# Optimization experiments

Hardware: AMD Instinct MI355X
Metric: run time of the kernel (lower is better)

Reference implementation:

```python
import jax, jax.numpy as jnp
import numpy as np

RES = 16          # grid resolution per axis -> num_models = 4096
L_XYZ = 10        # xyz positional-encoding frequencies -> input_ch = 63
L_DIR = 4         # dir positional-encoding frequencies -> input_ch_views = 27
W = 32
N_RAYS, N_SAMPLES = 1024, 128
NM = RES * RES * RES


def _embed(x, L):
    # NeRF frequency encoding: [x, sin(2^k x), cos(2^k x)] for k in 0..L-1
    freqs = 2.0 ** jnp.arange(L, dtype=x.dtype)          # (L,)
    xf = x[..., None, :] * freqs[:, None]                # (N, L, 3)
    enc = jnp.concatenate([jnp.sin(xf), jnp.cos(xf)], axis=-1)
    return jnp.concatenate([x, enc.reshape(x.shape[0], -1)], axis=-1)


def setup_inputs() -> dict:
    key = jax.random.key(0)
    ks = jax.random.split(key, 16)
    s = 0.05
    pts = jax.random.uniform(ks[0], (N_RAYS, N_SAMPLES, 3), dtype=jnp.float32)
    vd = jax.random.normal(ks[1], (N_RAYS, 3), dtype=jnp.float32)
    vd = vd / jnp.linalg.norm(vd, axis=-1, keepdims=True)
    return {
        "pts": pts,
        "viewdirs": vd,
        "pts_w0": s * jax.random.normal(ks[2], (NM, W, 63), dtype=jnp.float32),
        "pts_b0": s * jax.random.normal(ks[3], (NM, W), dtype=jnp.float32),
        "pts_w1": s * jax.random.normal(ks[4], (NM, W, W), dtype=jnp.float32),
        "pts_b1": s * jax.random.normal(ks[5], (NM, W), dtype=jnp.float32),
        "feat_w": s * jax.random.normal(ks[6], (NM, W, W), dtype=jnp.float32),
        "feat_b": s * jax.random.normal(ks[7], (NM, W), dtype=jnp.float32),
        "sigma_w": s * jax.random.normal(ks[8], (NM, 1, W), dtype=jnp.float32),
        "sigma_b": s * jax.random.normal(ks[9], (NM, 1), dtype=jnp.float32),
        "view_w": s * jax.random.normal(ks[10], (NM, W, W + 27), dtype=jnp.float32),
        "view_b": s * jax.random.normal(ks[11], (NM, W), dtype=jnp.float32),
        "rgb_w": s * jax.random.normal(ks[12], (NM, 3, W), dtype=jnp.float32),
        "rgb_b": s * jax.random.normal(ks[13], (NM, 3), dtype=jnp.float32),
    }


def reference(pts, viewdirs, pts_w0, pts_b0, pts_w1, pts_b1, feat_w, feat_b,
              sigma_w, sigma_b, view_w, view_b, rgb_w, rgb_b):
    n_rays, n_samples, _ = pts.shape
    p = pts.reshape(-1, 3)                                        # (N, 3)
    v = jnp.broadcast_to(viewdirs[:, None, :],
                         (n_rays, n_samples, 3)).reshape(-1, 3)   # (N, 3)

    # voxel index (aabb = [0,1]^3)
    scaled = jnp.clip(p * RES, 0.0, RES - 1.0)
    i3 = scaled.astype(jnp.int32)
    idx = i3[:, 0] * (RES * RES) + i3[:, 1] * RES + i3[:, 2]      # (N,)

    ep = _embed(p, L_XYZ)                                         # (N, 63)
    ev = _embed(v, L_DIR)                                         # (N, 27)

    # per-point tiny MLP with gathered weights: h @ w^T + b
    h = jax.nn.relu(jnp.einsum('nd,nod->no', ep, pts_w0[idx]) + pts_b0[idx])
    h = jax.nn.relu(jnp.einsum('nd,nod->no', h, pts_w1[idx]) + pts_b1[idx])

    sigma = jnp.einsum('nd,nod->no', h, sigma_w[idx]) + sigma_b[idx]   # (N, 1)
    feat = jnp.einsum('nd,nod->no', h, feat_w[idx]) + feat_b[idx]      # (N, W)

    h2 = jnp.concatenate([feat, ev], axis=-1)                          # (N, W+27)
    h2 = jax.nn.relu(jnp.einsum('nd,nod->no', h2, view_w[idx]) + view_b[idx])
    rgb = jnp.einsum('nd,nod->no', h2, rgb_w[idx]) + rgb_b[idx]        # (N, 3)

    out = jnp.concatenate([rgb, sigma], axis=-1).reshape(n_rays, n_samples, 4)
    return out[..., :3], out[..., 3:4]
```

## Files before the change

kernel.cpp:

```cpp
#include <hip/hip_runtime.h>

#define NM    4096
#define NPTS  131072
#define CAP   128

typedef _Float16 h8 __attribute__((ext_vector_type(8)));
typedef _Float16 h2 __attribute__((ext_vector_type(2)));
typedef float    f4 __attribute__((ext_vector_type(4)));
typedef int      i4 __attribute__((ext_vector_type(4)));

#define MF(a, b, c) __builtin_amdgcn_mfma_f32_16x16x32_f16((a), (b), (c), 0, 0, 0)

#if __has_builtin(__builtin_amdgcn_global_load_lds)
#define USE_DMA 1
#else
#define USE_DMA 0
#endif

static __device__ inline h2 pk(float a, float b) {
    return __builtin_bit_cast(h2, __builtin_amdgcn_cvt_pkrtz(a, b));
}

static __device__ inline h8 pack8(float u0, float u1, float u2, float u3,
                                  float u4, float u5, float u6, float u7) {
    i4 t;
    t[0] = __builtin_bit_cast(int, pk(u0, u1));
    t[1] = __builtin_bit_cast(int, pk(u2, u3));
    t[2] = __builtin_bit_cast(int, pk(u4, u5));
    t[3] = __builtin_bit_cast(int, pk(u6, u7));
    return __builtin_bit_cast(h8, t);
}

static __device__ inline h8 lds_row8(const float* __restrict__ X, int base,
                                     int d0, int lim) {
    float u[8];
    #pragma unroll
    for (int jj = 0; jj < 8; jj++) {
        int d = d0 + jj;
        float raw = X[base + d];
        u[jj] = (d < lim) ? raw : 0.f;
    }
    return pack8(u[0], u[1], u[2], u[3], u[4], u[5], u[6], u[7]);
}

static __device__ inline h8 lds_row8a(const float* __restrict__ X, int off) {
    f4 v0 = *(const f4*)(X + off);
    f4 v1 = *(const f4*)(X + off + 4);
    return pack8(v0[0], v0[1], v0[2], v0[3], v1[0], v1[1], v1[2], v1[3]);
}

static __device__ inline h8 load_row8(const float* __restrict__ rb, int d0, int lim) {
    float u[8];
    #pragma unroll
    for (int jj = 0; jj < 8; jj++) {
        int d = d0 + jj;
        u[jj] = (d < lim) ? rb[d] : 0.f;
    }
    return pack8(u[0], u[1], u[2], u[3], u[4], u[5], u[6], u[7]);
}

static __device__ inline float encdim(int d, int lim, float x, float y, float z) {
    int tt = d - 3;
    int k  = tt / 6;
    int r  = tt - 6 * k;
    float p = x;
    p = (r == 1 || r == 4) ? y : p;
    p = (r == 2 || r == 5) ? z : p;
    float f   = __int_as_float((k + 127) << 23);
    float arg = p * f + ((r >= 3) ? 1.57079632679f : 0.f);
    float sv  = __sinf(arg);
    float raw = (d == 0) ? x : ((d == 1) ? y : z);
    float val = (d < 3) ? raw : sv;
    return (d < lim) ? val : 0.f;
}

static __device__ inline h8 makeB(f4 d0, f4 d1, int quad, int col) {
    int laneA = ((quad & 1) * 2) * 16 + col;
    int laneB = laneA + 16;
    float a0 = __shfl(d0[0], laneA), b0 = __shfl(d1[0], laneA);
    float a1 = __shfl(d0[1], laneA), b1 = __shfl(d1[1], laneA);
    float a2 = __shfl(d0[2], laneA), b2 = __shfl(d1[2], laneA);
    float a3 = __shfl(d0[3], laneA), b3 = __shfl(d1[3], laneA);
    float a4 = __shfl(d0[0], laneB), b4 = __shfl(d1[0], laneB);
    float a5 = __shfl(d0[1], laneB), b5 = __shfl(d1[1], laneB);
    float a6 = __shfl(d0[2], laneB), b6 = __shfl(d1[2], laneB);
    float a7 = __shfl(d0[3], laneB), b7 = __shfl(d1[3], laneB);
    bool hi = quad >= 2;
    return pack8(hi ? b0 : a0, hi ? b1 : a1, hi ? b2 : a2, hi ? b3 : a3,
                 hi ? b4 : a4, hi ? b5 : a5, hi ? b6 : a6, hi ? b7 : a7);
}

static __device__ inline f4 relu4(f4 a) {
    f4 r;
    r[0] = fmaxf(a[0], 0.f); r[1] = fmaxf(a[1], 0.f);
    r[2] = fmaxf(a[2], 0.f); r[3] = fmaxf(a[3], 0.f);
    return r;
}

#if USE_DMA
static __device__ inline void dma16(const float* g, const float* l) {
    __builtin_amdgcn_global_load_lds(
        (const __attribute__((address_space(1))) void*)g,
        (__attribute__((address_space(3))) void*)l, 16, 0, 0);
}
#endif

__global__ __launch_bounds__(256) void k_bucket(const float* __restrict__ pts,
                                                int* __restrict__ count,
                                                int* __restrict__ plist) {
    int n = blockIdx.x * 256 + threadIdx.x;
    if (n >= NPTS) return;
    float x = pts[3 * n + 0], y = pts[3 * n + 1], z = pts[3 * n + 2];
    int ix = (int)fminf(fmaxf(x * 16.f, 0.f), 15.f);
    int iy = (int)fminf(fmaxf(y * 16.f, 0.f), 15.f);
    int iz = (int)fminf(fmaxf(z * 16.f, 0.f), 15.f);
    int v = (ix << 8) | (iy << 4) | iz;
    int pos = atomicAdd(&count[v], 1);
    if (pos < CAP) plist[v * CAP + pos] = n;
}

__global__ __launch_bounds__(256) void k_mlp(
    const float* __restrict__ pts, const float* __restrict__ vds,
    const float* __restrict__ w0g, const float* __restrict__ b0g,
    const float* __restrict__ w1g, const float* __restrict__ b1g,
    const float* __restrict__ fwg, const float* __restrict__ fbg,
    const float* __restrict__ swg, const float* __restrict__ sbg,
    const float* __restrict__ vwg, const float* __restrict__ vbg,
    const float* __restrict__ rwg, const float* __restrict__ rbg,
    const int* __restrict__ count, const int* __restrict__ plist,
    float* __restrict__ out) {
    __shared__ __align__(16) float X[4][3040];

    const int t    = threadIdx.x;
    const int wid  = t >> 6;
    const int lane = t & 63;
    const int col  = lane & 15;
    const int quad = lane >> 4;
    const int k8   = quad * 8;
    const int v    = blockIdx.x * 4 + wid;
    const int c    = min(count[v], CAP);
    if (c == 0) return;
    float* Xw = X[wid];

#if USE_DMA
    {
        const float* g = w0g + (size_t)v * 2016;
        #pragma unroll
        for (int k = 0; k < 7; k++) dma16(g + k * 256 + lane * 4, Xw + k * 256);
        if (lane < 56) dma16(g + 1792 + lane * 4, Xw + 1792);
        const float* g1 = w1g + (size_t)v * 1024;
        #pragma unroll
        for (int k = 0; k < 4; k++) dma16(g1 + k * 256 + lane * 4, Xw + 2016 + k * 256);
    }
#endif

    int ncur = plist[v * CAP + min(col, c - 1)];
    float px = pts[3 * ncur], py = pts[3 * ncur + 1], pz = pts[3 * ncur + 2];
    int ray = ncur >> 7;
    float dx = vds[3 * ray], dy = vds[3 * ray + 1], dz = vds[3 * ray + 2];

    f4 cB0[2], cB1[2], cFB[2], cVB[2];
    #pragma unroll
    for (int Ti = 0; Ti < 2; Ti++) {
        int ro = v * 32 + Ti * 16 + quad * 4;
        cB0[Ti] = *(const f4*)(b0g + ro);
        cB1[Ti] = *(const f4*)(b1g + ro);
        cFB[Ti] = *(const f4*)(fbg + ro);
        cVB[Ti] = *(const f4*)(vbg + ro);
    }
    const float rb0 = rbg[v * 3 + 0], rb1 = rbg[v * 3 + 1], rb2 = rbg[v * 3 + 2];
    const float sb  = sbg[v];

    h8 bE0, bE1, bD;
    auto encode = [&](float qx, float qy, float qz, float ex, float ey, float ez) {
        bE0 = pack8(encdim(k8 + 0, 63, qx, qy, qz), encdim(k8 + 1, 63, qx, qy, qz),
                    encdim(k8 + 2, 63, qx, qy, qz), encdim(k8 + 3, 63, qx, qy, qz),
                    encdim(k8 + 4, 63, qx, qy, qz), encdim(k8 + 5, 63, qx, qy, qz),
                    encdim(k8 + 6, 63, qx, qy, qz), encdim(k8 + 7, 63, qx, qy, qz));
        bE1 = pack8(encdim(32 + k8 + 0, 63, qx, qy, qz), encdim(32 + k8 + 1, 63, qx, qy, qz),
                    encdim(32 + k8 + 2, 63, qx, qy, qz), encdim(32 + k8 + 3, 63, qx, qy, qz),
                    encdim(32 + k8 + 4, 63, qx, qy, qz), encdim(32 + k8 + 5, 63, qx, qy, qz),
                    encdim(32 + k8 + 6, 63, qx, qy, qz), encdim(32 + k8 + 7, 63, qx, qy, qz));
        bD  = pack8(encdim(k8 + 0, 27, ex, ey, ez), encdim(k8 + 1, 27, ex, ey, ez),
                    encdim(k8 + 2, 27, ex, ey, ez), encdim(k8 + 3, 27, ex, ey, ez),
                    encdim(k8 + 4, 27, ex, ey, ez), encdim(k8 + 5, 27, ex, ey, ez),
                    encdim(k8 + 6, 27, ex, ey, ez), encdim(k8 + 7, 27, ex, ey, ez));
    };
    encode(px, py, pz, dx, dy, dz);

    h8 aW0[2][2], aW1[2], aVW[2][2], aFW[2], aSG, aRGB;

#if USE_DMA
    asm volatile("s_waitcnt vmcnt(0)" ::: "memory");
    __builtin_amdgcn_sched_barrier(0);
    #pragma unroll
    for (int Ti = 0; Ti < 2; Ti++) {
        int r0 = (Ti * 16 + col) * 63;
        aW0[Ti][0] = lds_row8(Xw, r0, k8, 63);
        aW0[Ti][1] = lds_row8(Xw, r0, 32 + k8, 63);
        aW1[Ti] = lds_row8a(Xw, 2016 + (Ti * 16 + col) * 32 + k8);
    }
    asm volatile("s_waitcnt lgkmcnt(0)" ::: "memory");
    __builtin_amdgcn_sched_barrier(0);

    {
        const float* g = vwg + (size_t)v * 1888;
        #pragma unroll
        for (int k = 0; k < 7; k++) dma16(g + k * 256 + lane * 4, Xw + k * 256);
        if (lane < 24) dma16(g + 1792 + lane * 4, Xw + 1792);
        const float* g1 = fwg + (size_t)v * 1024;
        #pragma unroll
        for (int k = 0; k < 4; k++) dma16(g1 + k * 256 + lane * 4, Xw + 1888 + k * 256);
        if (lane < 8)  dma16(swg + (size_t)v * 32 + lane * 4, Xw + 2912);
        if (lane < 24) dma16(rwg + (size_t)v * 96 + lane * 4, Xw + 2944);
    }
#else
    {
        #pragma unroll
        for (int Ti = 0; Ti < 2; Ti++) {
            const float* rb = w0g + (size_t)v * 2016 + (Ti * 16 + col) * 63;
            aW0[Ti][0] = load_row8(rb, k8, 63);
            aW0[Ti][1] = load_row8(rb, 32 + k8, 63);
            aW1[Ti] = load_row8(w1g + (size_t)v * 1024 + (Ti * 16 + col) * 32, k8, 32);
        }
    }
#endif

    const f4 z4 = {0.f, 0.f, 0.f, 0.f};

    f4 d0 = MF(aW0[0][0], bE0, cB0[0]); d0 = MF(aW0[0][1], bE1, d0);
    f4 d1 = MF(aW0[1][0], bE0, cB0[1]); d1 = MF(aW0[1][1], bE1, d1);
    d0 = relu4(d0); d1 = relu4(d1);
    h8 bH = makeB(d0, d1, quad, col);
    f4 e0 = MF(aW1[0], bH, cB1[0]);
    f4 e1 = MF(aW1[1], bH, cB1[1]);
    e0 = relu4(e0); e1 = relu4(e1);
    h8 bG = makeB(e0, e1, quad, col);

#if USE_DMA
    asm volatile("s_waitcnt vmcnt(0)" ::: "memory");
    __builtin_amdgcn_sched_barrier(0);
    #pragma unroll
    for (int Ti = 0; Ti < 2; Ti++) {
        int r1 = (Ti * 16 + col) * 59;
        aVW[Ti][0] = lds_row8(Xw, r1, k8, 59);
        aVW[Ti][1] = lds_row8(Xw, r1, 32 + k8, 59);
        aFW[Ti] = lds_row8a(Xw, 1888 + (Ti * 16 + col) * 32 + k8);
    }
    aSG  = (col == 0) ? lds_row8a(Xw, 2912 + k8) : h8{};
    aRGB = (col < 3) ? lds_row8a(Xw, 2944 + col * 32 + k8) : h8{};
#else
    {
        #pragma unroll
        for (int Ti = 0; Ti < 2; Ti++) {
            const float* rb = vwg + (size_t)v * 1888 + (Ti * 16 + col) * 59;
            aVW[Ti][0] = load_row8(rb, k8, 59);
            aVW[Ti][1] = load_row8(rb, 32 + k8, 59);
            aFW[Ti] = load_row8(fwg + (size_t)v * 1024 + (Ti * 16 + col) * 32, k8, 32);
        }
        aSG  = (col == 0) ? load_row8(swg + (size_t)v * 32, k8, 32) : h8{};
        aRGB = (col < 3) ? load_row8(rwg + (size_t)v * 96 + col * 32, k8, 32) : h8{};
    }
#endif

    {
        f4 s  = MF(aSG, bG, z4);
        f4 f0 = MF(aFW[0], bG, cFB[0]);
        f4 f1 = MF(aFW[1], bG, cFB[1]);
        h8 bF = makeB(f0, f1, quad, col);
        f4 v0 = MF(aVW[0][0], bF, cVB[0]); v0 = MF(aVW[0][1], bD, v0);
        f4 v1 = MF(aVW[1][0], bF, cVB[1]); v1 = MF(aVW[1][1], bD, v1);
        v0 = relu4(v0); v1 = relu4(v1);
        h8 bV = makeB(v0, v1, quad, col);
        f4 o  = MF(aRGB, bV, z4);
        if (quad == 0 && col < c) {
            out[3 * ncur + 0] = o[0] + rb0;
            out[3 * ncur + 1] = o[1] + rb1;
            out[3 * ncur + 2] = o[2] + rb2;
            out[3 * NPTS + ncur] = s[0] + sb;
        }
    }

    for (int base = 16; base < c; base += 16) {
        int n = plist[v * CAP + min(base + col, c - 1)];
        const bool active = (base + col) < c;
        float qx = pts[3 * n], qy = pts[3 * n + 1], qz = pts[3 * n + 2];
        int r2 = n >> 7;
        float ex = vds[3 * r2], ey = vds[3 * r2 + 1], ez = vds[3 * r2 + 2];
        encode(qx, qy, qz, ex, ey, ez);

        d0 = MF(aW0[0][0], bE0, cB0[0]); d0 = MF(aW0[0][1], bE1, d0);
        d1 = MF(aW0[1][0], bE0, cB0[1]); d1 = MF(aW0[1][1], bE1, d1);
        d0 = relu4(d0); d1 = relu4(d1);
        bH = makeB(d0, d1, quad, col);

        e0 = MF(aW1[0], bH, cB1[0]);
        e1 = MF(aW1[1], bH, cB1[1]);
        e0 = relu4(e0); e1 = relu4(e1);
        bG = makeB(e0, e1, quad, col);

        f4 s  = MF(aSG, bG, z4);
        f4 f0 = MF(aFW[0], bG, cFB[0]);
        f4 f1 = MF(aFW[1], bG, cFB[1]);
        h8 bF = makeB(f0, f1, quad, col);

        f4 v0 = MF(aVW[0][0], bF, cVB[0]); v0 = MF(aVW[0][1], bD, v0);
        f4 v1 = MF(aVW[1][0], bF, cVB[1]); v1 = MF(aVW[1][1], bD, v1);
        v0 = relu4(v0); v1 = relu4(v1);
        h8 bV = makeB(v0, v1, quad, col);
        f4 o  = MF(aRGB, bV, z4);

        if (quad == 0 && active) {
            out[3 * n + 0] = o[0] + rb0;
            out[3 * n + 1] = o[1] + rb1;
            out[3 * n + 2] = o[2] + rb2;
            out[3 * NPTS + n] = s[0] + sb;
        }
    }
}

extern "C" void kernel_launch(void* const* d_in, const int* in_sizes, int n_in,
                              void* d_out, int out_size, void* d_ws, size_t ws_size,
                              hipStream_t stream) {
    const float* pts = (const float*)d_in[0];
    const float* vds = (const float*)d_in[1];
    const float* w0  = (const float*)d_in[2];
    const float* b0  = (const float*)d_in[3];
    const float* w1  = (const float*)d_in[4];
    const float* b1  = (const float*)d_in[5];
    const float* fw  = (const float*)d_in[6];
    const float* fb  = (const float*)d_in[7];
    const float* sw  = (const float*)d_in[8];
    const float* sb  = (const float*)d_in[9];
    const float* vw  = (const float*)d_in[10];
    const float* vb  = (const float*)d_in[11];
    const float* rw  = (const float*)d_in[12];
    const float* rb  = (const float*)d_in[13];
    float* out = (float*)d_out;

    int* count = (int*)d_ws;
    int* plist = (int*)((char*)d_ws + NM * sizeof(int));

    (void)hipMemsetAsync(count, 0, NM * sizeof(int), stream);
    k_bucket<<<NPTS / 256, 256, 0, stream>>>(pts, count, plist);
    k_mlp<<<NM / 4, 256, 0, stream>>>(pts, vds, w0, b0, w1, b1, fw, fb, sw, sb,
                                      vw, vb, rw, rb, count, plist, out);
}
```

Measured before the change: 169.4 us.

## Use one-wave blocks per voxel, preload point list, prefetch next chunk's points

Each voxel now gets its own 64-thread block with a private LDS weight buffer, instead of four voxels packed into one 256-thread block. The voxel's point-index list is loaded once into registers and handed out per chunk with wave shuffles. The next 16-point chunk's coordinates and view directions are prefetched while the current chunk is being computed. The aim is to hide gather latency and let waves retire independently, at the cost of four times as many blocks and some extra registers for the prefetched values.

```diff
diff --git a/kernel.cpp b/kernel.cpp
--- a/kernel.cpp
+++ b/kernel.cpp
@@ -119,7 +119,7 @@
     if (pos < CAP) plist[v * CAP + pos] = n;
 }
 
-__global__ __launch_bounds__(256) void k_mlp(
+__global__ __launch_bounds__(64) void k_mlp(
     const float* __restrict__ pts, const float* __restrict__ vds,
     const float* __restrict__ w0g, const float* __restrict__ b0g,
     const float* __restrict__ w1g, const float* __restrict__ b1g,
@@ -129,35 +129,36 @@
     const float* __restrict__ rwg, const float* __restrict__ rbg,
     const int* __restrict__ count, const int* __restrict__ plist,
     float* __restrict__ out) {
-    __shared__ __align__(16) float X[4][3040];
-
-    const int t    = threadIdx.x;
-    const int wid  = t >> 6;
-    const int lane = t & 63;
+    __shared__ __align__(16) float X[3040];
+
+    const int lane = threadIdx.x & 63;
     const int col  = lane & 15;
     const int quad = lane >> 4;
     const int k8   = quad * 8;
-    const int v    = blockIdx.x * 4 + wid;
+    const int v    = blockIdx.x;
     const int c    = min(count[v], CAP);
     if (c == 0) return;
-    float* Xw = X[wid];
 
 #if USE_DMA
     {
         const float* g = w0g + (size_t)v * 2016;
         #pragma unroll
-        for (int k = 0; k < 7; k++) dma16(g + k * 256 + lane * 4, Xw + k * 256);
-        if (lane < 56) dma16(g + 1792 + lane * 4, Xw + 1792);
+        for (int k = 0; k < 7; k++) dma16(g + k * 256 + lane * 4, X + k * 256);
+        if (lane < 56) dma16(g + 1792 + lane * 4, X + 1792);
         const float* g1 = w1g + (size_t)v * 1024;
         #pragma unroll
-        for (int k = 0; k < 4; k++) dma16(g1 + k * 256 + lane * 4, Xw + 2016 + k * 256);
-    }
-#endif
-
-    int ncur = plist[v * CAP + min(col, c - 1)];
-    float px = pts[3 * ncur], py = pts[3 * ncur + 1], pz = pts[3 * ncur + 2];
-    int ray = ncur >> 7;
-    float dx = vds[3 * ray], dy = vds[3 * ray + 1], dz = vds[3 * ray + 2];
+        for (int k = 0; k < 4; k++) dma16(g1 + k * 256 + lane * 4, X + 2016 + k * 256);
+    }
+#endif
+
+    const int prow0 = plist[v * CAP + lane];
+    const int prow1 = plist[v * CAP + 64 + lane];
+    auto chunk_idx = [&](int base) -> int {
+        int e = min(base + col, c - 1);
+        int a = __shfl(prow0, e);
+        int b = __shfl(prow1, e - 64);
+        return (e < 64) ? a : b;
+    };
 
     f4 cB0[2], cB1[2], cFB[2], cVB[2];
     #pragma unroll
@@ -171,20 +172,34 @@
     const float rb0 = rbg[v * 3 + 0], rb1 = rbg[v * 3 + 1], rb2 = rbg[v * 3 + 2];
     const float sb  = sbg[v];
 
+    int ncur = chunk_idx(0);
+    float px = pts[3 * ncur], py = pts[3 * ncur + 1], pz = pts[3 * ncur + 2];
+    int ray = ncur >> 7;
+    float dx = vds[3 * ray], dy = vds[3 * ray + 1], dz = vds[3 * ray + 2];
+
+    int nnxt = 0;
+    float qx = 0.f, qy = 0.f, qz = 0.f, ex = 0.f, ey = 0.f, ez = 0.f;
+    if (16 < c) {
+        nnxt = chunk_idx(16);
+        qx = pts[3 * nnxt]; qy = pts[3 * nnxt + 1]; qz = pts[3 * nnxt + 2];
+        int r2 = nnxt >> 7;
+        ex = vds[3 * r2]; ey = vds[3 * r2 + 1]; ez = vds[3 * r2 + 2];
+    }
+
     h8 bE0, bE1, bD;
-    auto encode = [&](float qx, float qy, float qz, float ex, float ey, float ez) {
-        bE0 = pack8(encdim(k8 + 0, 63, qx, qy, qz), encdim(k8 + 1, 63, qx, qy, qz),
-                    encdim(k8 + 2, 63, qx, qy, qz), encdim(k8 + 3, 63, qx, qy, qz),
-                    encdim(k8 + 4, 63, qx, qy, qz), encdim(k8 + 5, 63, qx, qy, qz),
-                    encdim(k8 + 6, 63, qx, qy, qz), encdim(k8 + 7, 63, qx, qy, qz));
-        bE1 = pack8(encdim(32 + k8 + 0, 63, qx, qy, qz), encdim(32 + k8 + 1, 63, qx, qy, qz),
-                    encdim(32 + k8 + 2, 63, qx, qy, qz), encdim(32 + k8 + 3, 63, qx, qy, qz),
-                    encdim(32 + k8 + 4, 63, qx, qy, qz), encdim(32 + k8 + 5, 63, qx, qy, qz),
-                    encdim(32 + k8 + 6, 63, qx, qy, qz), encdim(32 + k8 + 7, 63, qx, qy, qz));
-        bD  = pack8(encdim(k8 + 0, 27, ex, ey, ez), encdim(k8 + 1, 27, ex, ey, ez),
-                    encdim(k8 + 2, 27, ex, ey, ez), encdim(k8 + 3, 27, ex, ey, ez),
-                    encdim(k8 + 4, 27, ex, ey, ez), encdim(k8 + 5, 27, ex, ey, ez),
-                    encdim(k8 + 6, 27, ex, ey, ez), encdim(k8 + 7, 27, ex, ey, ez));
+    auto encode = [&](float sx, float sy, float sz, float tx, float ty, float tz) {
+        bE0 = pack8(encdim(k8 + 0, 63, sx, sy, sz), encdim(k8 + 1, 63, sx, sy, sz),
+                    encdim(k8 + 2, 63, sx, sy, sz), encdim(k8 + 3, 63, sx, sy, sz),
+                    encdim(k8 + 4, 63, sx, sy, sz), encdim(k8 + 5, 63, sx, sy, sz),
+                    encdim(k8 + 6, 63, sx, sy, sz), encdim(k8 + 7, 63, sx, sy, sz));
+        bE1 = pack8(encdim(32 + k8 + 0, 63, sx, sy, sz), encdim(32 + k8 + 1, 63, sx, sy, sz),
+                    encdim(32 + k8 + 2, 63, sx, sy, sz), encdim(32 + k8 + 3, 63, sx, sy, sz),
+                    encdim(32 + k8 + 4, 63, sx, sy, sz), encdim(32 + k8 + 5, 63, sx, sy, sz),
+                    encdim(32 + k8 + 6, 63, sx, sy, sz), encdim(32 + k8 + 7, 63, sx, sy, sz));
+        bD  = pack8(encdim(k8 + 0, 27, tx, ty, tz), encdim(k8 + 1, 27, tx, ty, tz),
+                    encdim(k8 + 2, 27, tx, ty, tz), encdim(k8 + 3, 27, tx, ty, tz),
+                    encdim(k8 + 4, 27, tx, ty, tz), encdim(k8 + 5, 27, tx, ty, tz),
+                    encdim(k8 + 6, 27, tx, ty, tz), encdim(k8 + 7, 27, tx, ty, tz));
     };
     encode(px, py, pz, dx, dy, dz);
 
@@ -196,9 +211,9 @@
     #pragma unroll
     for (int Ti = 0; Ti < 2; Ti++) {
         int r0 = (Ti * 16 + col) * 63;
-        aW0[Ti][0] = lds_row8(Xw, r0, k8, 63);
-        aW0[Ti][1] = lds_row8(Xw, r0, 32 + k8, 63);
-        aW1[Ti] = lds_row8a(Xw, 2016 + (Ti * 16 + col) * 32 + k8);
+        aW0[Ti][0] = lds_row8(X, r0, k8, 63);
+        aW0[Ti][1] = lds_row8(X, r0, 32 + k8, 63);
+        aW1[Ti] = lds_row8a(X, 2016 + (Ti * 16 + col) * 32 + k8);
     }
     asm volatile("s_waitcnt lgkmcnt(0)" ::: "memory");
     __builtin_amdgcn_sched_barrier(0);
@@ -206,13 +221,13 @@
     {
         const float* g = vwg + (size_t)v * 1888;
         #pragma unroll
-        for (int k = 0; k < 7; k++) dma16(g + k * 256 + lane * 4, Xw + k * 256);
-        if (lane < 24) dma16(g + 1792 + lane * 4, Xw + 1792);
+        for (int k = 0; k < 7; k++) dma16(g + k * 256 + lane * 4, X + k * 256);
+        if (lane < 24) dma16(g + 1792 + lane * 4, X + 1792);
         const float* g1 = fwg + (size_t)v * 1024;
         #pragma unroll
-        for (int k = 0; k < 4; k++) dma16(g1 + k * 256 + lane * 4, Xw + 1888 + k * 256);
-        if (lane < 8)  dma16(swg + (size_t)v * 32 + lane * 4, Xw + 2912);
-        if (lane < 24) dma16(rwg + (size_t)v * 96 + lane * 4, Xw + 2944);
+        for (int k = 0; k < 4; k++) dma16(g1 + k * 256 + lane * 4, X + 1888 + k * 256);
+        if (lane < 8)  dma16(swg + (size_t)v * 32 + lane * 4, X + 2912);
+        if (lane < 24) dma16(rwg + (size_t)v * 96 + lane * 4, X + 2944);
     }
 #else
     {
@@ -243,12 +258,12 @@
     #pragma unroll
     for (int Ti = 0; Ti < 2; Ti++) {
         int r1 = (Ti * 16 + col) * 59;
-        aVW[Ti][0] = lds_row8(Xw, r1, k8, 59);
-        aVW[Ti][1] = lds_row8(Xw, r1, 32 + k8, 59);
-        aFW[Ti] = lds_row8a(Xw, 1888 + (Ti * 16 + col) * 32 + k8);
-    }
-    aSG  = (col == 0) ? lds_row8a(Xw, 2912 + k8) : h8{};
-    aRGB = (col < 3) ? lds_row8a(Xw, 2944 + col * 32 + k8) : h8{};
+        aVW[Ti][0] = lds_row8(X, r1, k8, 59);
+        aVW[Ti][1] = lds_row8(X, r1, 32 + k8, 59);
+        aFW[Ti] = lds_row8a(X, 1888 + (Ti * 16 + col) * 32 + k8);
+    }
+    aSG  = (col == 0) ? lds_row8a(X, 2912 + k8) : h8{};
+    aRGB = (col < 3) ? lds_row8a(X, 2944 + col * 32 + k8) : h8{};
 #else
     {
         #pragma unroll
@@ -282,12 +297,18 @@
     }
 
     for (int base = 16; base < c; base += 16) {
-        int n = plist[v * CAP + min(base + col, c - 1)];
-        const bool active = (base + col) < c;
-        float qx = pts[3 * n], qy = pts[3 * n + 1], qz = pts[3 * n + 2];
-        int r2 = n >> 7;
-        float ex = vds[3 * r2], ey = vds[3 * r2 + 1], ez = vds[3 * r2 + 2];
-        encode(qx, qy, qz, ex, ey, ez);
+        const int n = nnxt;
+        const float cx = qx, cy = qy, cz = qz;
+        const float fx = ex, fy = ey, fz = ez;
+
+        if (base + 16 < c) {
+            nnxt = chunk_idx(base + 16);
+            qx = pts[3 * nnxt]; qy = pts[3 * nnxt + 1]; qz = pts[3 * nnxt + 2];
+            int r2 = nnxt >> 7;
+            ex = vds[3 * r2]; ey = vds[3 * r2 + 1]; ez = vds[3 * r2 + 2];
+        }
+
+        encode(cx, cy, cz, fx, fy, fz);
 
         d0 = MF(aW0[0][0], bE0, cB0[0]); d0 = MF(aW0[0][1], bE1, d0);
         d1 = MF(aW0[1][0], bE0, cB0[1]); d1 = MF(aW0[1][1], bE1, d1);
@@ -310,7 +331,7 @@
         h8 bV = makeB(v0, v1, quad, col);
         f4 o  = MF(aRGB, bV, z4);
 
-        if (quad == 0 && active) {
+        if (quad == 0 && (base + col) < c) {
             out[3 * n + 0] = o[0] + rb0;
             out[3 * n + 1] = o[1] + rb1;
             out[3 * n + 2] = o[2] + rb2;
@@ -343,6 +364,6 @@
 
     (void)hipMemsetAsync(count, 0, NM * sizeof(int), stream);
     k_bucket<<<NPTS / 256, 256, 0, stream>>>(pts, count, plist);
-    k_mlp<<<NM / 4, 256, 0, stream>>>(pts, vds, w0, b0, w1, b1, fw, fb, sw, sb,
-                                      vw, vb, rw, rb, count, plist, out);
-}
+    k_mlp<<<NM, 64, 0, stream>>>(pts, vds, w0, b0, w1, b1, fw, fb, sw, sb,
+                                 vw, vb, rw, rb, count, plist, out);
+}
```

Result: faster. 165.3 us (-2.4%).
